# Optimization experiments

Measured on AMD Instinct MI355X. Metric: run time of the kernel, lower is better.

The kernel has to match this reference:

```python
import jax, jax.numpy as jnp
import numpy as np

B = 4096
INPUT_SIZE = 256
LATENT = 64
HIDDEN = 512
ACTIONS = 12
EXPERTS = 8
GATE_H = 128
IN_DIM = INPUT_SIZE + LATENT      # 320, first-layer expert in-dim
INTER = HIDDEN + LATENT           # 576, later-layer expert in-dim


def _lip_linear_params(key, out_f, in_f):
    kw, kb = jax.random.split(key)
    stdv = 1.0 / np.sqrt(in_f)
    W = jax.random.uniform(kw, (out_f, in_f), jnp.float32, -stdv, stdv)
    b = jax.random.uniform(kb, (out_f,), jnp.float32, -stdv, stdv)
    c = jnp.abs(W).sum(1).max()[None]  # shape (1,), matches init
    return W, b, c


def _expert_params(key, e, in_f, out_f):
    # kaiming_uniform_ on tensor of shape (E, in, out): fan_in computed by torch
    kw = key
    gain = np.sqrt(2.0)  # default a=sqrt(5) -> gain = sqrt(2/(1+5)) ... torch uses a=math.sqrt(5)? no: default a=0
    # torch.nn.init.kaiming_uniform_(weight) default a=0, fan_in = in*out? torch computes fan from dims[1:]
    fan_in = in_f
    bound = np.sqrt(6.0 / fan_in)
    W = jax.random.uniform(kw, (e, in_f, out_f), jnp.float32, -bound, bound)
    b = jnp.full((e, out_f), 0.01, jnp.float32)
    return W, b


def setup_inputs() -> dict:
    key = jax.random.key(0)
    ks = jax.random.split(key, 10)
    z = jax.random.normal(ks[0], (B, LATENT), jnp.float32)
    c = jax.random.normal(ks[1], (B, INPUT_SIZE), jnp.float32)
    w0, b0 = _expert_params(ks[2], EXPERTS, IN_DIM, HIDDEN)
    w1, b1 = _expert_params(ks[3], EXPERTS, INTER, HIDDEN)
    w2, b2 = _expert_params(ks[4], EXPERTS, INTER, ACTIONS)
    gw0, gb0, gc0 = _lip_linear_params(ks[5], GATE_H, IN_DIM)
    gw1, gb1, gc1 = _lip_linear_params(ks[6], GATE_H, GATE_H)
    gw2, gb2, gc2 = _lip_linear_params(ks[7], EXPERTS, GATE_H)
    return {"z": z, "c": c, "w0": w0, "b0": b0, "w1": w1, "b1": b1,
            "w2": w2, "b2": b2, "gw0": gw0, "gb0": gb0, "gc0": gc0,
            "gw1": gw1, "gb1": gb1, "gc1": gc1, "gw2": gw2, "gb2": gb2, "gc2": gc2}


def _lip_linear(x, W, b, cc):
    # LipschitzLinear: scale rows of W so row-wise L1 norm <= softplus(c)
    lipc = jax.nn.softplus(cc)                      # (1,)
    scale = jnp.minimum(lipc / jnp.abs(W).sum(1), 1.0)  # (out,)
    return x @ (W * scale[:, None]).T + b


def _moe_forward(z, c, coeff, layers):
    layer_out = c
    for W, bias, act in layers:
        inp = jnp.concatenate([z, layer_out], axis=1)       # (B, in)
        # per-expert GEMM then coefficient mix: avoids (B,in,out) intermediate
        h = jnp.einsum('bi,eio->beo', inp, W)               # (B, E, out)
        out = jnp.einsum('be,beo->bo', coeff, h) + coeff @ bias
        layer_out = jax.nn.elu(out) if act else out
    return layer_out


def reference(z, c, w0, b0, w1, b1, w2, b2,
              gw0, gb0, gc0, gw1, gb1, gc1, gw2, gb2, gc2):
    x = jnp.concatenate([z, c], axis=1)
    h = jax.nn.elu(_lip_linear(x, gw0, gb0, gc0))
    h = jax.nn.elu(_lip_linear(h, gw1, gb1, gc1))
    logits = _lip_linear(h, gw2, gb2, gc2)
    coeff = jax.nn.softmax(logits, axis=1)                  # (B, E)
    layers = [(w0, b0, True), (w1, b1, True), (w2, b2, False)]
    return _moe_forward(z, c, coeff, layers)
```

## Files before the change

kernel.cpp:

```cpp
#include <hip/hip_runtime.h>
#include <hip/hip_bf16.h>
#include <hip/hip_fp16.h>
#include <math.h>

#define BATCH 4096
#define INPUT_SIZE 256
#define LATENT 64
#define HIDDEN 512
#define ACTIONS 12
#define EXPERTS 8
#define GATE_H 128
#define IN_DIM (INPUT_SIZE + LATENT)
#define INTER (HIDDEN + LATENT)

typedef unsigned int u32;
typedef unsigned short u16;
typedef __attribute__((ext_vector_type(8))) short short8;
typedef __attribute__((ext_vector_type(8))) _Float16 f16x8;
typedef __attribute__((ext_vector_type(16))) float f32x16;

__device__ __forceinline__ u16 f2h(float x) { return __half_as_ushort(__float2half(x)); }
__device__ __forceinline__ float h2f(u16 u) { return __half2float(__ushort_as_half(u)); }

__device__ __forceinline__ void gload16(const void* g, void* lds) {
    __builtin_amdgcn_global_load_lds(
        (const __attribute__((address_space(1))) u32*)g,
        (__attribute__((address_space(3))) u32*)lds, 16, 0, 0);
}

#define GS 4
__global__ __launch_bounds__(256) void gate_forward_v4(
    const float* __restrict__ z, const float* __restrict__ c,
    const float* __restrict__ W0t, const float* __restrict__ b0,
    const float* __restrict__ W1t, const float* __restrict__ b1,
    const float* __restrict__ W2t, const float* __restrict__ b2,
    float* __restrict__ coeff) {
    __shared__ float xs[GS][IN_DIM + 2];
    __shared__ float hq[4][GS][GATE_H];
    __shared__ float h1[GS][GATE_H + 1];
    __shared__ float h2[GS][GATE_H + 1];
    __shared__ float red[GS][EXPERTS];

    const int b4 = blockIdx.x * GS;
    const int t = threadIdx.x;
    const int np = t & 63, kq = t >> 6;
    const int n0 = np * 2;

    for (int idx = t; idx < GS * IN_DIM; idx += 256) {
        const int s = idx / IN_DIM, i = idx - s * IN_DIM;
        xs[s][i] = (i < LATENT) ? z[(size_t)(b4 + s) * LATENT + i]
                                : c[(size_t)(b4 + s) * INPUT_SIZE + (i - LATENT)];
    }
    __syncthreads();

    {
        float a0[GS], a1[GS];
        #pragma unroll
        for (int s = 0; s < GS; ++s) { a0[s] = 0.f; a1[s] = 0.f; }
        const int i0 = kq * 80;
        #pragma unroll 8
        for (int i = i0; i < i0 + 80; ++i) {
            const float2 wv2 = *(const float2*)(W0t + (size_t)i * GATE_H + n0);
            #pragma unroll
            for (int s = 0; s < GS; ++s) {
                a0[s] = fmaf(xs[s][i], wv2.x, a0[s]);
                a1[s] = fmaf(xs[s][i], wv2.y, a1[s]);
            }
        }
        #pragma unroll
        for (int s = 0; s < GS; ++s) { hq[kq][s][n0] = a0[s]; hq[kq][s][n0 + 1] = a1[s]; }
    }
    __syncthreads();
    if (kq == 0) {
        #pragma unroll
        for (int s = 0; s < GS; ++s)
            #pragma unroll
            for (int j = 0; j < 2; ++j) {
                const int n = n0 + j;
                const float v = b0[n] + hq[0][s][n] + hq[1][s][n] + hq[2][s][n] + hq[3][s][n];
                h1[s][n] = v > 0.f ? v : expm1f(v);
            }
    }
    __syncthreads();

    {
        float a0[GS], a1[GS];
        #pragma unroll
        for (int s = 0; s < GS; ++s) { a0[s] = 0.f; a1[s] = 0.f; }
        const int i0 = kq * 32;
        #pragma unroll 8
        for (int i = i0; i < i0 + 32; ++i) {
            const float2 wv2 = *(const float2*)(W1t + (size_t)i * GATE_H + n0);
            #pragma unroll
            for (int s = 0; s < GS; ++s) {
                a0[s] = fmaf(h1[s][i], wv2.x, a0[s]);
                a1[s] = fmaf(h1[s][i], wv2.y, a1[s]);
            }
        }
        #pragma unroll
        for (int s = 0; s < GS; ++s) { hq[kq][s][n0] = a0[s]; hq[kq][s][n0 + 1] = a1[s]; }
    }
    __syncthreads();
    if (kq == 0) {
        #pragma unroll
        for (int s = 0; s < GS; ++s)
            #pragma unroll
            for (int j = 0; j < 2; ++j) {
                const int n = n0 + j;
                const float v = b1[n] + hq[0][s][n] + hq[1][s][n] + hq[2][s][n] + hq[3][s][n];
                h2[s][n] = v > 0.f ? v : expm1f(v);
            }
    }
    __syncthreads();

    if (t < GS * EXPERTS) {
        const int s = t >> 3, e = t & 7;
        float acc = b2[e];
        #pragma unroll 8
        for (int i = 0; i < GATE_H; ++i)
            acc = fmaf(h2[s][i], W2t[(size_t)i * EXPERTS + e], acc);
        red[s][e] = acc;
    }
    __syncthreads();
    if (t < GS) {
        float m = red[t][0];
        #pragma unroll
        for (int i = 1; i < EXPERTS; ++i) m = fmaxf(m, red[t][i]);
        float e[EXPERTS];
        float sum = 0.f;
        #pragma unroll
        for (int i = 0; i < EXPERTS; ++i) { e[i] = expf(red[t][i] - m); sum += e[i]; }
        const float inv = 1.f / sum;
        #pragma unroll
        for (int i = 0; i < EXPERTS; ++i)
            coeff[(size_t)(b4 + t) * EXPERTS + i] = e[i] * inv;
    }
}

__global__ __launch_bounds__(256) void pack_all_kernel(
    const float* __restrict__ w0, const float* __restrict__ w1,
    const float* __restrict__ w2,
    const float* __restrict__ z, const float* __restrict__ c,
    u16* __restrict__ Bpk0, u16* __restrict__ Bpk1, u16* __restrict__ Bpk2,
    u16* __restrict__ Apk0, u16* __restrict__ Apk1, u16* __restrict__ Apk2,
    const float* __restrict__ gw0, const float* __restrict__ gc0,
    const float* __restrict__ gw1, const float* __restrict__ gc1,
    const float* __restrict__ gw2, const float* __restrict__ gc2,
    float* __restrict__ gW0t, float* __restrict__ gW1t, float* __restrict__ gW2t) {
    const int t = threadIdx.x, wv = t >> 6, l = t & 63;
    const int x = blockIdx.x, y = blockIdx.y;

    if (y < 33) {
        __shared__ float tile[4][16][33];
        const float* w; u16* Bpk; int IN, OUT, nblk;
        if (y < 16)      { w = w0; Bpk = Bpk0; IN = IN_DIM; OUT = HIDDEN;  nblk = y; }
        else if (y < 32) { w = w1; Bpk = Bpk1; IN = INTER;  OUT = HIDDEN;  nblk = y - 16; }
        else             { w = w2; Bpk = Bpk2; IN = INTER;  OUT = ACTIONS; nblk = 0; }
        const int NK = IN / 16;
        const int e = x, n0 = nblk * 32;
        const int col = l & 31, half = l >> 5;
        char* base = (char*)Bpk + ((size_t)(nblk * EXPERTS + e) * NK) * 1024;

        for (int jj = wv; jj < NK; jj += 4) {
            #pragma unroll
            for (int i = 0; i < 8; ++i) {
                const int r = i * 2 + half;
                float v = 0.f;
                if (n0 + col < OUT) v = w[((size_t)e * IN + jj * 16 + r) * OUT + n0 + col];
                tile[wv][r][col] = v;
            }
            short8 hh;
            #pragma unroll
            for (int i = 0; i < 8; ++i)
                hh[i] = (short)f2h(tile[wv][half * 8 + i][col]);
            *(short8*)(base + (size_t)jj * 1024 + l * 16) = hh;
        }
    } else if (y < 49) {
        constexpr int NK0 = 20, NK1 = 36;
        const int bblk = (y - 33) * 8 + x;
        const int r = l & 31, half = l >> 5;
        const int row = bblk * 32 + r;
        char* base0 = (char*)Apk0 + (size_t)bblk * NK0 * 1024;
        char* base1 = (char*)Apk1 + (size_t)bblk * NK1 * 1024;
        char* base2 = (char*)Apk2 + (size_t)bblk * NK1 * 1024;

        for (int jj = wv; jj < NK0; jj += 4) {
            const int k = jj * 16 + half * 8;
            const float* src = (k < LATENT) ? (z + (size_t)row * LATENT + k)
                                            : (c + (size_t)row * INPUT_SIZE + (k - LATENT));
            short8 hh;
            #pragma unroll
            for (int i = 0; i < 8; ++i) hh[i] = (short)f2h(src[i]);
            *(short8*)(base0 + (size_t)jj * 1024 + l * 16) = hh;
            if (jj < 4) {
                *(short8*)(base1 + (size_t)jj * 1024 + l * 16) = hh;
                *(short8*)(base2 + (size_t)jj * 1024 + l * 16) = hh;
            }
        }
    } else {
        const int row_g = (y - 49) * 32 + x * 4 + wv;
        if (row_g < 264) {
            const float* W; const float* cc; float* Wt; int cols, rows, row;
            if (row_g < 128)      { W = gw0; cc = gc0; Wt = gW0t; cols = IN_DIM; rows = GATE_H; row = row_g; }
            else if (row_g < 256) { W = gw1; cc = gc1; Wt = gW1t; cols = GATE_H; rows = GATE_H; row = row_g - 128; }
            else                  { W = gw2; cc = gc2; Wt = gW2t; cols = GATE_H; rows = EXPERTS; row = row_g - 256; }
            const float* w = W + (size_t)row * cols;
            float s = 0.f;
            for (int i = l; i < cols; i += 64) s += fabsf(w[i]);
            #pragma unroll
            for (int off = 32; off > 0; off >>= 1) s += __shfl_down(s, off, 64);
            s = __shfl(s, 0, 64);
            const float cv = cc[0];
            const float lipc = (cv > 0.f) ? (cv + log1pf(expf(-cv))) : log1pf(expf(cv));
            const float scale = fminf(lipc / s, 1.0f);
            for (int i = l; i < cols; i += 64)
                Wt[(size_t)i * rows + row] = w[i] * scale;
        }
    }
}

template<int NPART>
__global__ __launch_bounds__(256) void reduce_pack_kernel(
    const u16* __restrict__ P16, const float* __restrict__ coeff,
    const float* __restrict__ bias, u16* __restrict__ ApkNext) {
    constexpr int NK = 36;
    __shared__ float biasS[EXPERTS][256];
    __shared__ float coeffS[32][9];
    const int t = threadIdx.x, wv = t >> 6, l = t & 63;
    const int bblk = blockIdx.x, ch = blockIdx.y;
    const int r = l & 31, half = l >> 5;
    const int row = bblk * 32 + r;

    for (int idx = t; idx < EXPERTS * 256; idx += 256)
        biasS[idx >> 8][idx & 255] = bias[(idx >> 8) * HIDDEN + ch * 256 + (idx & 255)];
    for (int idx = t; idx < 32 * 8; idx += 256)
        coeffS[idx >> 3][idx & 7] = coeff[(size_t)(bblk * 32 + (idx >> 3)) * 8 + (idx & 7)];
    __syncthreads();

    char* base = (char*)ApkNext + (size_t)bblk * NK * 1024;
    for (int jj = ch * 16 + wv; jj < ch * 16 + 16; jj += 4) {
        const int cb = jj * 16 + half * 8;
        float v[8];
        #pragma unroll
        for (int i = 0; i < 8; ++i) v[i] = 0.f;
        #pragma unroll
        for (int p = 0; p < NPART; ++p) {
            const short8 q = *(const short8*)(P16 + ((size_t)p * BATCH + row) * HIDDEN + cb);
            #pragma unroll
            for (int i = 0; i < 8; ++i) v[i] += h2f((u16)q[i]);
        }
        #pragma unroll
        for (int e = 0; e < EXPERTS; ++e) {
            const float cv = coeffS[r][e];
            #pragma unroll
            for (int i = 0; i < 8; ++i) v[i] = fmaf(cv, biasS[e][cb - ch * 256 + i], v[i]);
        }
        short8 hh;
        #pragma unroll
        for (int i = 0; i < 8; ++i) {
            const float hv = v[i] > 0.f ? v[i] : expm1f(v[i]);
            hh[i] = (short)f2h(hv);
        }
        *(short8*)(base + (size_t)(4 + jj) * 1024 + l * 16) = hh;
    }
}

__global__ __launch_bounds__(256) void reduce_out_kernel(
    const float* __restrict__ P2, const float* __restrict__ coeff,
    const float* __restrict__ b2, float* __restrict__ out) {
    const int t = threadIdx.x;
    const int bblk = blockIdx.x;
    for (int idx = t; idx < 32 * ACTIONS; idx += 256) {
        const int r = idx / ACTIONS, n = idx % ACTIONS;
        const int row = bblk * 32 + r;
        float s = 0.f;
        #pragma unroll
        for (int p = 0; p < 8; ++p) s += P2[((size_t)p * BATCH + row) * 32 + n];
        const float* cf = coeff + (size_t)row * 8;
        #pragma unroll
        for (int e = 0; e < 8; ++e) s = fmaf(cf[e], b2[e * ACTIONS + n], s);
        out[(size_t)row * ACTIONS + n] = s;
    }
}

template<int NK, bool F16P>
__global__ __launch_bounds__(512) void moe_gemm_big(
    const u16* __restrict__ Apk, const u16* __restrict__ Bpk,
    const float* __restrict__ coeff, void* __restrict__ Pout) {
    constexpr int TOT = NK / 4;

    __shared__ __align__(16) char As[3 * 16384];
    __shared__ float coeffT[2][128];

    const int t = threadIdx.x, wv = t >> 6, l = t & 63;
    const int wr = wv & 1, wc = wv >> 1;

    const int fid = blockIdx.x + 32 * (blockIdx.y + 4 * blockIdx.z);
    const int xcd = fid & 7, idx = fid >> 3;
    const int bx = xcd * 4 + (idx & 3);
    const int yz = idx >> 2;
    const int by = yz & 3, bz = yz >> 2;

    const int b0 = bx * 128;
    const int bblk0 = bx * 4;
    const int nblkg = by * 4 + wc;
    const int part = bz;
    const int estart = part * 2;

    for (int i2 = t; i2 < 2 * 128; i2 += 512)
        coeffT[i2 >> 7][i2 & 127] =
            coeff[(size_t)(b0 + (i2 & 127)) * EXPERTS + estart + (i2 >> 7)];

    const char* Ab = (const char*)Apk;
    const char* Bbase[2];
    #pragma unroll
    for (int e = 0; e < 2; ++e)
        Bbase[e] = (const char*)Bpk +
                   ((size_t)(nblkg * EXPERTS + estart + e) * NK) * 1024 + l * 16;

    f32x16 accE[2][2];
    accE[0][0] = (f32x16)0.f; accE[0][1] = (f32x16)0.f;
    accE[1][0] = (f32x16)0.f; accE[1][1] = (f32x16)0.f;

    f16x8 breg[2][2][4];

    auto stageA = [&](int s) {
        char* dst = As + (s % 3) * 16384;
        #pragma unroll
        for (int q = 0; q < 2; ++q) {
            const int cf = wv * 2 + q, bb = cf >> 2, kq = cf & 3;
            gload16(Ab + ((size_t)(bblk0 + bb) * NK + s * 4 + kq) * 1024 + l * 16,
                    dst + cf * 1024 + l * 16);
        }
    };

    __syncthreads();

    stageA(0);
    #pragma unroll
    for (int e = 0; e < 2; ++e)
        #pragma unroll
        for (int q = 0; q < 4; ++q)
            breg[0][e][q] = *(const f16x8*)(Bbase[e] + (size_t)q * 1024);
    stageA(1);
    #pragma unroll
    for (int e = 0; e < 2; ++e)
        #pragma unroll
        for (int q = 0; q < 4; ++q)
            breg[1][e][q] = *(const f16x8*)(Bbase[e] + (size_t)(4 + q) * 1024);

    #pragma unroll
    for (int s = 0; s < TOT; ++s) {
        if (s == TOT - 1) asm volatile("s_waitcnt vmcnt(0)" ::: "memory");
        else              asm volatile("s_waitcnt vmcnt(10)" ::: "memory");
        __builtin_amdgcn_sched_barrier(0);
        __builtin_amdgcn_s_barrier();
        __builtin_amdgcn_sched_barrier(0);

        if (s + 2 < TOT) stageA(s + 2);

        const char* buf = As + (s % 3) * 16384;
        f16x8 af0[4], af1[4];
        #pragma unroll
        for (int j = 0; j < 4; ++j) {
            af0[j] = *(const f16x8*)(buf + ((wr * 2 + 0) * 4 + j) * 1024 + l * 16);
            af1[j] = *(const f16x8*)(buf + ((wr * 2 + 1) * 4 + j) * 1024 + l * 16);
        }
        #pragma unroll
        for (int e = 0; e < 2; ++e)
            #pragma unroll
            for (int j = 0; j < 4; ++j) {
                accE[e][0] = __builtin_amdgcn_mfma_f32_32x32x16_f16(af0[j], breg[s & 1][e][j], accE[e][0], 0, 0, 0);
                accE[e][1] = __builtin_amdgcn_mfma_f32_32x32x16_f16(af1[j], breg[s & 1][e][j], accE[e][1], 0, 0, 0);
            }
        if (s + 2 < TOT) {
            #pragma unroll
            for (int e = 0; e < 2; ++e)
                #pragma unroll
                for (int q = 0; q < 4; ++q)
                    breg[s & 1][e][q] = *(const f16x8*)(Bbase[e] + (size_t)((s + 2) * 4 + q) * 1024);
        }
    }

    const int ncol = nblkg * 32 + (l & 31);
    #pragma unroll
    for (int m = 0; m < 2; ++m) {
        #pragma unroll
        for (int g = 0; g < 16; ++g) {
            const int rloc = (g & 3) + 8 * (g >> 2) + 4 * (l >> 5);
            const int row = wr * 64 + m * 32 + rloc;
            float v = coeffT[0][row] * accE[0][m][g] + coeffT[1][row] * accE[1][m][g];
            const size_t off = ((size_t)part * BATCH + b0 + row) * HIDDEN + ncol;
            if (F16P) ((u16*)Pout)[off] = f2h(v);
            else      ((float*)Pout)[off] = v;
        }
    }
}

template<int NK, int WN, int EPB, int OUTW, int GX, int GY, int GZ, bool F16P>
__global__ __launch_bounds__(128 * WN) void moe_gemm(
    const u16* __restrict__ Apk, const u16* __restrict__ Bpk,
    const float* __restrict__ coeff, void* __restrict__ Pout) {
    constexpr int TOT = NK / 4;
    constexpr int NWAVE = 2 * WN;
    constexpr int CPW = 16 / NWAVE;
    constexpr int CPX = GX / 8;

    __shared__ __align__(16) char As[3 * 16384];
    __shared__ float coeffT[EPB][128];

    const int t = threadIdx.x, wv = t >> 6, l = t & 63;
    const int wr = wv & 1, wc = wv >> 1;

    const int fid = blockIdx.x + GX * (blockIdx.y + GY * blockIdx.z);
    const int xcd = fid & 7, idx = fid >> 3;
    const int bx = xcd * CPX + (idx % CPX);
    const int yz = idx / CPX;
    const int by = yz % GY, bz = yz / GY;

    const int b0 = bx * 128;
    const int bblk0 = bx * 4;
    const int nblkg = by * WN + wc;
    const int part = bz;
    const int estart = part * EPB;

    for (int idx2 = t; idx2 < EPB * 128; idx2 += 128 * WN)
        coeffT[idx2 >> 7][idx2 & 127] =
            coeff[(size_t)(b0 + (idx2 & 127)) * EXPERTS + estart + (idx2 >> 7)];

    const char* Ab = (const char*)Apk;
    const char* Bbase[EPB];
    #pragma unroll
    for (int e = 0; e < EPB; ++e)
        Bbase[e] = (const char*)Bpk +
                   ((size_t)(nblkg * EXPERTS + estart + e) * NK) * 1024 + l * 16;

    f32x16 accE[EPB][2];
    #pragma unroll
    for (int e = 0; e < EPB; ++e) { accE[e][0] = (f32x16)0.f; accE[e][1] = (f32x16)0.f; }

    f16x8 breg[2][EPB][4];

    auto stageA = [&](int s) {
        char* dst = As + (s % 3) * 16384;
        #pragma unroll
        for (int q = 0; q < CPW; ++q) {
            const int cf = wv * CPW + q, bb = cf >> 2, kq = cf & 3;
            gload16(Ab + ((size_t)(bblk0 + bb) * NK + s * 4 + kq) * 1024 + l * 16,
                    dst + cf * 1024 + l * 16);
        }
    };

    __syncthreads();

    stageA(0);
    #pragma unroll
    for (int e = 0; e < EPB; ++e)
        #pragma unroll
        for (int q = 0; q < 4; ++q)
            breg[0][e][q] = *(const f16x8*)(Bbase[e] + (size_t)q * 1024);
    stageA(1);
    #pragma unroll
    for (int e = 0; e < EPB; ++e)
        #pragma unroll
        for (int q = 0; q < 4; ++q)
            breg[1][e][q] = *(const f16x8*)(Bbase[e] + (size_t)(4 + q) * 1024);

    #pragma unroll
    for (int s = 0; s < TOT; ++s) {
        if (s == TOT - 1) asm volatile("s_waitcnt vmcnt(0)" ::: "memory");
        else              asm volatile("s_waitcnt vmcnt(12)" ::: "memory");
        __builtin_amdgcn_sched_barrier(0);
        __builtin_amdgcn_s_barrier();
        __builtin_amdgcn_sched_barrier(0);

        if (s + 2 < TOT) stageA(s + 2);

        const char* buf = As + (s % 3) * 16384;
        f16x8 af0[4], af1[4];
        #pragma unroll
        for (int j = 0; j < 4; ++j) {
            af0[j] = *(const f16x8*)(buf + ((wr * 2 + 0) * 4 + j) * 1024 + l * 16);
            af1[j] = *(const f16x8*)(buf + ((wr * 2 + 1) * 4 + j) * 1024 + l * 16);
        }
        #pragma unroll
        for (int e = 0; e < EPB; ++e)
            #pragma unroll
            for (int j = 0; j < 4; ++j) {
                accE[e][0] = __builtin_amdgcn_mfma_f32_32x32x16_f16(af0[j], breg[s & 1][e][j], accE[e][0], 0, 0, 0);
                accE[e][1] = __builtin_amdgcn_mfma_f32_32x32x16_f16(af1[j], breg[s & 1][e][j], accE[e][1], 0, 0, 0);
            }
        if (s + 2 < TOT) {
            #pragma unroll
            for (int e = 0; e < EPB; ++e)
                #pragma unroll
                for (int q = 0; q < 4; ++q)
                    breg[s & 1][e][q] = *(const f16x8*)(Bbase[e] + (size_t)((s + 2) * 4 + q) * 1024);
        }
    }

    const int ncol = nblkg * 32 + (l & 31);
    #pragma unroll
    for (int m = 0; m < 2; ++m) {
        #pragma unroll
        for (int g = 0; g < 16; ++g) {
            const int rloc = (g & 3) + 8 * (g >> 2) + 4 * (l >> 5);
            const int row = wr * 64 + m * 32 + rloc;
            float v = 0.f;
            #pragma unroll
            for (int e = 0; e < EPB; ++e) v = fmaf(coeffT[e][row], accE[e][m][g], v);
            const size_t off = ((size_t)part * BATCH + b0 + row) * OUTW + ncol;
            if (F16P) ((u16*)Pout)[off] = f2h(v);
            else      ((float*)Pout)[off] = v;
        }
    }
}

extern "C" void kernel_launch(void* const* d_in, const int* in_sizes, int n_in,
                              void* d_out, int out_size, void* d_ws, size_t ws_size,
                              hipStream_t stream) {
    const float* z   = (const float*)d_in[0];
    const float* c   = (const float*)d_in[1];
    const float* w0  = (const float*)d_in[2];
    const float* b0  = (const float*)d_in[3];
    const float* w1  = (const float*)d_in[4];
    const float* b1  = (const float*)d_in[5];
    const float* w2  = (const float*)d_in[6];
    const float* b2  = (const float*)d_in[7];
    const float* gw0 = (const float*)d_in[8];
    const float* gb0 = (const float*)d_in[9];
    const float* gc0 = (const float*)d_in[10];
    const float* gw1 = (const float*)d_in[11];
    const float* gb1 = (const float*)d_in[12];
    const float* gc1 = (const float*)d_in[13];
    const float* gw2 = (const float*)d_in[14];
    const float* gb2 = (const float*)d_in[15];
    const float* gc2 = (const float*)d_in[16];
    float* out = (float*)d_out;

    char* p = (char*)d_ws;
    float* coeff = (float*)p;  p += (size_t)BATCH * EXPERTS * 4;
    float* gW0t  = (float*)p;  p += (size_t)GATE_H * IN_DIM * 4;
    float* gW1t  = (float*)p;  p += (size_t)GATE_H * GATE_H * 4;
    float* gW2t  = (float*)p;  p += (size_t)EXPERTS * GATE_H * 4;
    u16* Apk0 = (u16*)p;       p += (size_t)128 * 20 * 1024;
    u16* Apk1 = (u16*)p;       p += (size_t)128 * 36 * 1024;
    u16* Apk2 = (u16*)p;       p += (size_t)128 * 36 * 1024;
    u16* Bpk0 = (u16*)p;       p += (size_t)16 * 8 * 20 * 1024;
    u16* Bpk1 = (u16*)p;       p += (size_t)16 * 8 * 36 * 1024;
    u16* Bpk2 = (u16*)p;       p += (size_t)8 * 36 * 1024;
    u16* P16  = (u16*)p;       p += (size_t)4 * BATCH * HIDDEN * 2;
    float* P32 = (float*)P16;

    pack_all_kernel<<<dim3(8, 58), 256, 0, stream>>>(
        w0, w1, w2, z, c, Bpk0, Bpk1, Bpk2, Apk0, Apk1, Apk2,
        gw0, gc0, gw1, gc1, gw2, gc2, gW0t, gW1t, gW2t);

    gate_forward_v4<<<BATCH / GS, 256, 0, stream>>>(z, c, gW0t, gb0, gW1t, gb1,
                                                    gW2t, gb2, coeff);

    moe_gemm_big<20, true><<<dim3(32, 4, 4), 512, 0, stream>>>(
        Apk0, Bpk0, coeff, P16);
    reduce_pack_kernel<4><<<dim3(128, 2), 256, 0, stream>>>(P16, coeff, b0, Apk1);

    moe_gemm_big<36, true><<<dim3(32, 4, 4), 512, 0, stream>>>(
        Apk1, Bpk1, coeff, P16);
    reduce_pack_kernel<4><<<dim3(128, 2), 256, 0, stream>>>(P16, coeff, b1, Apk2);

    moe_gemm<36, 1, 1, 32, 32, 1, 8, false><<<dim3(32, 1, 8), 128, 0, stream>>>(
        Apk2, Bpk2, coeff, P32);
    reduce_out_kernel<<<128, 256, 0, stream>>>(P32, coeff, b2, out);
}
```

Before: 118.3 us.

## Fuse split-K partial reductions into GEMM kernels via last-block atomic counters

Removes the separate reduce_pack and reduce_out kernels. Each GEMM block now writes its partial, bumps an atomic counter for its tile, and the last arriving block sums the partials, adds the bias, applies ELU and packs the next layer's input. The layer GEMM grid is reshaped to 256-thread blocks with twice as many N tiles. This cuts kernel launches and inter-kernel gaps, at the cost of threadfences, atomics and a serial reduction tail in the last block of each tile. The counters are zeroed by an extra row of pack_all_kernel.

```diff
diff --git a/kernel.cpp b/kernel.cpp
--- a/kernel.cpp
+++ b/kernel.cpp
@@ -146,7 +146,8 @@
     const float* __restrict__ gw0, const float* __restrict__ gc0,
     const float* __restrict__ gw1, const float* __restrict__ gc1,
     const float* __restrict__ gw2, const float* __restrict__ gc2,
-    float* __restrict__ gW0t, float* __restrict__ gW1t, float* __restrict__ gW2t) {
+    float* __restrict__ gW0t, float* __restrict__ gW1t, float* __restrict__ gW2t,
+    int* __restrict__ ctrs) {
     const int t = threadIdx.x, wv = t >> 6, l = t & 63;
     const int x = blockIdx.x, y = blockIdx.y;
 
@@ -197,7 +198,7 @@
                 *(short8*)(base2 + (size_t)jj * 1024 + l * 16) = hh;
             }
         }
-    } else {
+    } else if (y < 58) {
         const int row_g = (y - 49) * 32 + x * 4 + wv;
         if (row_g < 264) {
             const float* W; const float* cc; float* Wt; int cols, rows, row;
@@ -216,98 +217,39 @@
             for (int i = l; i < cols; i += 64)
                 Wt[(size_t)i * rows + row] = w[i] * scale;
         }
+    } else {
+        if (x == 0) for (int i = t; i < 544; i += 256) ctrs[i] = 0;
     }
 }
 
-template<int NPART>
-__global__ __launch_bounds__(256) void reduce_pack_kernel(
-    const u16* __restrict__ P16, const float* __restrict__ coeff,
-    const float* __restrict__ bias, u16* __restrict__ ApkNext) {
-    constexpr int NK = 36;
-    __shared__ float biasS[EXPERTS][256];
-    __shared__ float coeffS[32][9];
-    const int t = threadIdx.x, wv = t >> 6, l = t & 63;
-    const int bblk = blockIdx.x, ch = blockIdx.y;
-    const int r = l & 31, half = l >> 5;
-    const int row = bblk * 32 + r;
-
-    for (int idx = t; idx < EXPERTS * 256; idx += 256)
-        biasS[idx >> 8][idx & 255] = bias[(idx >> 8) * HIDDEN + ch * 256 + (idx & 255)];
-    for (int idx = t; idx < 32 * 8; idx += 256)
-        coeffS[idx >> 3][idx & 7] = coeff[(size_t)(bblk * 32 + (idx >> 3)) * 8 + (idx & 7)];
-    __syncthreads();
-
-    char* base = (char*)ApkNext + (size_t)bblk * NK * 1024;
-    for (int jj = ch * 16 + wv; jj < ch * 16 + 16; jj += 4) {
-        const int cb = jj * 16 + half * 8;
-        float v[8];
-        #pragma unroll
-        for (int i = 0; i < 8; ++i) v[i] = 0.f;
-        #pragma unroll
-        for (int p = 0; p < NPART; ++p) {
-            const short8 q = *(const short8*)(P16 + ((size_t)p * BATCH + row) * HIDDEN + cb);
-            #pragma unroll
-            for (int i = 0; i < 8; ++i) v[i] += h2f((u16)q[i]);
-        }
-        #pragma unroll
-        for (int e = 0; e < EXPERTS; ++e) {
-            const float cv = coeffS[r][e];
-            #pragma unroll
-            for (int i = 0; i < 8; ++i) v[i] = fmaf(cv, biasS[e][cb - ch * 256 + i], v[i]);
-        }
-        short8 hh;
-        #pragma unroll
-        for (int i = 0; i < 8; ++i) {
-            const float hv = v[i] > 0.f ? v[i] : expm1f(v[i]);
-            hh[i] = (short)f2h(hv);
-        }
-        *(short8*)(base + (size_t)(4 + jj) * 1024 + l * 16) = hh;
-    }
-}
-
-__global__ __launch_bounds__(256) void reduce_out_kernel(
-    const float* __restrict__ P2, const float* __restrict__ coeff,
-    const float* __restrict__ b2, float* __restrict__ out) {
-    const int t = threadIdx.x;
-    const int bblk = blockIdx.x;
-    for (int idx = t; idx < 32 * ACTIONS; idx += 256) {
-        const int r = idx / ACTIONS, n = idx % ACTIONS;
-        const int row = bblk * 32 + r;
-        float s = 0.f;
-        #pragma unroll
-        for (int p = 0; p < 8; ++p) s += P2[((size_t)p * BATCH + row) * 32 + n];
-        const float* cf = coeff + (size_t)row * 8;
-        #pragma unroll
-        for (int e = 0; e < 8; ++e) s = fmaf(cf[e], b2[e * ACTIONS + n], s);
-        out[(size_t)row * ACTIONS + n] = s;
-    }
-}
-
-template<int NK, bool F16P>
-__global__ __launch_bounds__(512) void moe_gemm_big(
+template<int NK>
+__global__ __launch_bounds__(256) void moe_gemm_rp(
     const u16* __restrict__ Apk, const u16* __restrict__ Bpk,
-    const float* __restrict__ coeff, void* __restrict__ Pout) {
+    const float* __restrict__ coeff, const float* __restrict__ bias,
+    u16* __restrict__ P16, u16* __restrict__ ApkNext, int* __restrict__ ctr) {
     constexpr int TOT = NK / 4;
+    constexpr int GX = 32, GY = 8, GZ = 4;
 
     __shared__ __align__(16) char As[3 * 16384];
     __shared__ float coeffT[2][128];
+    __shared__ int tick;
 
     const int t = threadIdx.x, wv = t >> 6, l = t & 63;
     const int wr = wv & 1, wc = wv >> 1;
 
-    const int fid = blockIdx.x + 32 * (blockIdx.y + 4 * blockIdx.z);
+    const int fid = blockIdx.x + GX * (blockIdx.y + GY * blockIdx.z);
     const int xcd = fid & 7, idx = fid >> 3;
-    const int bx = xcd * 4 + (idx & 3);
-    const int yz = idx >> 2;
-    const int by = yz & 3, bz = yz >> 2;
+    const int bx = xcd * 4 + (idx % 4);
+    const int yz = idx / 4;
+    const int by = yz % GY, bz = yz / GY;
 
     const int b0 = bx * 128;
     const int bblk0 = bx * 4;
-    const int nblkg = by * 4 + wc;
+    const int nblkg = by * 2 + wc;
     const int part = bz;
     const int estart = part * 2;
 
-    for (int i2 = t; i2 < 2 * 128; i2 += 512)
+    for (int i2 = t; i2 < 2 * 128; i2 += 256)
         coeffT[i2 >> 7][i2 & 127] =
             coeff[(size_t)(b0 + (i2 & 127)) * EXPERTS + estart + (i2 >> 7)];
 
@@ -327,8 +269,8 @@
     auto stageA = [&](int s) {
         char* dst = As + (s % 3) * 16384;
         #pragma unroll
-        for (int q = 0; q < 2; ++q) {
-            const int cf = wv * 2 + q, bb = cf >> 2, kq = cf & 3;
+        for (int q = 0; q < 4; ++q) {
+            const int cf = wv * 4 + q, bb = cf >> 2, kq = cf & 3;
             gload16(Ab + ((size_t)(bblk0 + bb) * NK + s * 4 + kq) * 1024 + l * 16,
                     dst + cf * 1024 + l * 16);
         }
@@ -345,123 +287,6 @@
     stageA(1);
     #pragma unroll
     for (int e = 0; e < 2; ++e)
-        #pragma unroll
-        for (int q = 0; q < 4; ++q)
-            breg[1][e][q] = *(const f16x8*)(Bbase[e] + (size_t)(4 + q) * 1024);
-
-    #pragma unroll
-    for (int s = 0; s < TOT; ++s) {
-        if (s == TOT - 1) asm volatile("s_waitcnt vmcnt(0)" ::: "memory");
-        else              asm volatile("s_waitcnt vmcnt(10)" ::: "memory");
-        __builtin_amdgcn_sched_barrier(0);
-        __builtin_amdgcn_s_barrier();
-        __builtin_amdgcn_sched_barrier(0);
-
-        if (s + 2 < TOT) stageA(s + 2);
-
-        const char* buf = As + (s % 3) * 16384;
-        f16x8 af0[4], af1[4];
-        #pragma unroll
-        for (int j = 0; j < 4; ++j) {
-            af0[j] = *(const f16x8*)(buf + ((wr * 2 + 0) * 4 + j) * 1024 + l * 16);
-            af1[j] = *(const f16x8*)(buf + ((wr * 2 + 1) * 4 + j) * 1024 + l * 16);
-        }
-        #pragma unroll
-        for (int e = 0; e < 2; ++e)
-            #pragma unroll
-            for (int j = 0; j < 4; ++j) {
-                accE[e][0] = __builtin_amdgcn_mfma_f32_32x32x16_f16(af0[j], breg[s & 1][e][j], accE[e][0], 0, 0, 0);
-                accE[e][1] = __builtin_amdgcn_mfma_f32_32x32x16_f16(af1[j], breg[s & 1][e][j], accE[e][1], 0, 0, 0);
-            }
-        if (s + 2 < TOT) {
-            #pragma unroll
-            for (int e = 0; e < 2; ++e)
-                #pragma unroll
-                for (int q = 0; q < 4; ++q)
-                    breg[s & 1][e][q] = *(const f16x8*)(Bbase[e] + (size_t)((s + 2) * 4 + q) * 1024);
-        }
-    }
-
-    const int ncol = nblkg * 32 + (l & 31);
-    #pragma unroll
-    for (int m = 0; m < 2; ++m) {
-        #pragma unroll
-        for (int g = 0; g < 16; ++g) {
-            const int rloc = (g & 3) + 8 * (g >> 2) + 4 * (l >> 5);
-            const int row = wr * 64 + m * 32 + rloc;
-            float v = coeffT[0][row] * accE[0][m][g] + coeffT[1][row] * accE[1][m][g];
-            const size_t off = ((size_t)part * BATCH + b0 + row) * HIDDEN + ncol;
-            if (F16P) ((u16*)Pout)[off] = f2h(v);
-            else      ((float*)Pout)[off] = v;
-        }
-    }
-}
-
-template<int NK, int WN, int EPB, int OUTW, int GX, int GY, int GZ, bool F16P>
-__global__ __launch_bounds__(128 * WN) void moe_gemm(
-    const u16* __restrict__ Apk, const u16* __restrict__ Bpk,
-    const float* __restrict__ coeff, void* __restrict__ Pout) {
-    constexpr int TOT = NK / 4;
-    constexpr int NWAVE = 2 * WN;
-    constexpr int CPW = 16 / NWAVE;
-    constexpr int CPX = GX / 8;
-
-    __shared__ __align__(16) char As[3 * 16384];
-    __shared__ float coeffT[EPB][128];
-
-    const int t = threadIdx.x, wv = t >> 6, l = t & 63;
-    const int wr = wv & 1, wc = wv >> 1;
-
-    const int fid = blockIdx.x + GX * (blockIdx.y + GY * blockIdx.z);
-    const int xcd = fid & 7, idx = fid >> 3;
-    const int bx = xcd * CPX + (idx % CPX);
-    const int yz = idx / CPX;
-    const int by = yz % GY, bz = yz / GY;
-
-    const int b0 = bx * 128;
-    const int bblk0 = bx * 4;
-    const int nblkg = by * WN + wc;
-    const int part = bz;
-    const int estart = part * EPB;
-
-    for (int idx2 = t; idx2 < EPB * 128; idx2 += 128 * WN)
-        coeffT[idx2 >> 7][idx2 & 127] =
-            coeff[(size_t)(b0 + (idx2 & 127)) * EXPERTS + estart + (idx2 >> 7)];
-
-    const char* Ab = (const char*)Apk;
-    const char* Bbase[EPB];
-    #pragma unroll
-    for (int e = 0; e < EPB; ++e)
-        Bbase[e] = (const char*)Bpk +
-                   ((size_t)(nblkg * EXPERTS + estart + e) * NK) * 1024 + l * 16;
-
-    f32x16 accE[EPB][2];
-    #pragma unroll
-    for (int e = 0; e < EPB; ++e) { accE[e][0] = (f32x16)0.f; accE[e][1] = (f32x16)0.f; }
-
-    f16x8 breg[2][EPB][4];
-
-    auto stageA = [&](int s) {
-        char* dst = As + (s % 3) * 16384;
-        #pragma unroll
-        for (int q = 0; q < CPW; ++q) {
-            const int cf = wv * CPW + q, bb = cf >> 2, kq = cf & 3;
-            gload16(Ab + ((size_t)(bblk0 + bb) * NK + s * 4 + kq) * 1024 + l * 16,
-                    dst + cf * 1024 + l * 16);
-        }
-    };
-
-    __syncthreads();
-
-    stageA(0);
-    #pragma unroll
-    for (int e = 0; e < EPB; ++e)
-        #pragma unroll
-        for (int q = 0; q < 4; ++q)
-            breg[0][e][q] = *(const f16x8*)(Bbase[e] + (size_t)q * 1024);
-    stageA(1);
-    #pragma unroll
-    for (int e = 0; e < EPB; ++e)
         #pragma unroll
         for (int q = 0; q < 4; ++q)
             breg[1][e][q] = *(const f16x8*)(Bbase[e] + (size_t)(4 + q) * 1024);
@@ -484,7 +309,7 @@
             af1[j] = *(const f16x8*)(buf + ((wr * 2 + 1) * 4 + j) * 1024 + l * 16);
         }
         #pragma unroll
-        for (int e = 0; e < EPB; ++e)
+        for (int e = 0; e < 2; ++e)
             #pragma unroll
             for (int j = 0; j < 4; ++j) {
                 accE[e][0] = __builtin_amdgcn_mfma_f32_32x32x16_f16(af0[j], breg[s & 1][e][j], accE[e][0], 0, 0, 0);
@@ -492,7 +317,7 @@
             }
         if (s + 2 < TOT) {
             #pragma unroll
-            for (int e = 0; e < EPB; ++e)
+            for (int e = 0; e < 2; ++e)
                 #pragma unroll
                 for (int q = 0; q < 4; ++q)
                     breg[s & 1][e][q] = *(const f16x8*)(Bbase[e] + (size_t)((s + 2) * 4 + q) * 1024);
@@ -506,13 +331,165 @@
         for (int g = 0; g < 16; ++g) {
             const int rloc = (g & 3) + 8 * (g >> 2) + 4 * (l >> 5);
             const int row = wr * 64 + m * 32 + rloc;
-            float v = 0.f;
-            #pragma unroll
-            for (int e = 0; e < EPB; ++e) v = fmaf(coeffT[e][row], accE[e][m][g], v);
-            const size_t off = ((size_t)part * BATCH + b0 + row) * OUTW + ncol;
-            if (F16P) ((u16*)Pout)[off] = f2h(v);
-            else      ((float*)Pout)[off] = v;
-        }
+            float v = coeffT[0][row] * accE[0][m][g] + coeffT[1][row] * accE[1][m][g];
+            P16[((size_t)part * BATCH + b0 + row) * HIDDEN + ncol] = f2h(v);
+        }
+    }
+
+    __threadfence();
+    __syncthreads();
+    if (t == 0) tick = atomicAdd(&ctr[bx * GY + by], 1);
+    __syncthreads();
+    if (tick != GZ - 1) return;
+    __threadfence();
+
+    float* coeffS = (float*)As;
+    float* biasS  = (float*)As + 128 * 8;
+    for (int i = t; i < 128 * 8; i += 256)
+        coeffS[i] = coeff[(size_t)(b0 + (i >> 3)) * 8 + (i & 7)];
+    for (int i = t; i < 8 * 64; i += 256)
+        biasS[i] = bias[(i >> 6) * HIDDEN + by * 64 + (i & 63)];
+    __syncthreads();
+
+    const int r = l & 31, half = l >> 5;
+    const int bblk = bblk0 + wv;
+    const int row = bblk * 32 + r;
+    const int rl8 = (wv * 32 + r) * 8;
+    char* basep = (char*)ApkNext + (size_t)bblk * 36 * 1024;
+    #pragma unroll
+    for (int jj2 = 0; jj2 < 4; ++jj2) {
+        const int jj = by * 4 + jj2;
+        const int cb = jj * 16 + half * 8;
+        float v[8];
+        #pragma unroll
+        for (int i = 0; i < 8; ++i) v[i] = 0.f;
+        #pragma unroll
+        for (int p = 0; p < GZ; ++p) {
+            const short8 q = *(const short8*)(P16 + ((size_t)p * BATCH + row) * HIDDEN + cb);
+            #pragma unroll
+            for (int i = 0; i < 8; ++i) v[i] += h2f((u16)q[i]);
+        }
+        const int cl = cb - by * 64;
+        #pragma unroll
+        for (int e = 0; e < EXPERTS; ++e) {
+            const float cv = coeffS[rl8 + e];
+            #pragma unroll
+            for (int i = 0; i < 8; ++i) v[i] = fmaf(cv, biasS[e * 64 + cl + i], v[i]);
+        }
+        short8 hh;
+        #pragma unroll
+        for (int i = 0; i < 8; ++i) {
+            const float hv = v[i] > 0.f ? v[i] : expm1f(v[i]);
+            hh[i] = (short)f2h(hv);
+        }
+        *(short8*)(basep + (size_t)(4 + jj) * 1024 + l * 16) = hh;
+    }
+}
+
+__global__ __launch_bounds__(128) void moe_gemm_l2f(
+    const u16* __restrict__ Apk, const u16* __restrict__ Bpk,
+    const float* __restrict__ coeff, const float* __restrict__ b2,
+    float* __restrict__ P32, float* __restrict__ out, int* __restrict__ ctr) {
+    constexpr int NK = 36, TOT = 9, GX = 32, GZ = 8;
+
+    __shared__ __align__(16) char As[3 * 16384];
+    __shared__ float coeffT[128];
+    __shared__ int tick;
+
+    const int t = threadIdx.x, wv = t >> 6, l = t & 63;
+    const int wr = wv & 1;
+
+    const int fid = blockIdx.x + GX * blockIdx.z;
+    const int xcd = fid & 7, idx = fid >> 3;
+    const int bx = xcd * 4 + (idx % 4);
+    const int part = idx / 4;
+
+    const int b0 = bx * 128;
+    const int bblk0 = bx * 4;
+
+    for (int i2 = t; i2 < 128; i2 += 128)
+        coeffT[i2] = coeff[(size_t)(b0 + i2) * EXPERTS + part];
+
+    const char* Ab = (const char*)Apk;
+    const char* Bb = (const char*)Bpk + ((size_t)part * NK) * 1024 + l * 16;
+
+    f32x16 accE[2];
+    accE[0] = (f32x16)0.f; accE[1] = (f32x16)0.f;
+
+    f16x8 breg[2][4];
+
+    auto stageA = [&](int s) {
+        char* dst = As + (s % 3) * 16384;
+        #pragma unroll
+        for (int q = 0; q < 8; ++q) {
+            const int cf = wv * 8 + q, bb = cf >> 2, kq = cf & 3;
+            gload16(Ab + ((size_t)(bblk0 + bb) * NK + s * 4 + kq) * 1024 + l * 16,
+                    dst + cf * 1024 + l * 16);
+        }
+    };
+    auto bload = [&](int s, int set) {
+        #pragma unroll
+        for (int q = 0; q < 4; ++q)
+            breg[set][q] = *(const f16x8*)(Bb + (size_t)(s * 4 + q) * 1024);
+    };
+
+    __syncthreads();
+    stageA(0); bload(0, 0);
+    stageA(1); bload(1, 1);
+
+    #pragma unroll
+    for (int s = 0; s < TOT; ++s) {
+        if (s == TOT - 1) asm volatile("s_waitcnt vmcnt(0)" ::: "memory");
+        else              asm volatile("s_waitcnt vmcnt(12)" ::: "memory");
+        __builtin_amdgcn_sched_barrier(0);
+        __builtin_amdgcn_s_barrier();
+        __builtin_amdgcn_sched_barrier(0);
+
+        if (s + 2 < TOT) stageA(s + 2);
+
+        const char* buf = As + (s % 3) * 16384;
+        f16x8 af0[4], af1[4];
+        #pragma unroll
+        for (int j = 0; j < 4; ++j) {
+            af0[j] = *(const f16x8*)(buf + ((wr * 2 + 0) * 4 + j) * 1024 + l * 16);
+            af1[j] = *(const f16x8*)(buf + ((wr * 2 + 1) * 4 + j) * 1024 + l * 16);
+        }
+        #pragma unroll
+        for (int j = 0; j < 4; ++j) {
+            accE[0] = __builtin_amdgcn_mfma_f32_32x32x16_f16(af0[j], breg[s & 1][j], accE[0], 0, 0, 0);
+            accE[1] = __builtin_amdgcn_mfma_f32_32x32x16_f16(af1[j], breg[s & 1][j], accE[1], 0, 0, 0);
+        }
+        if (s + 2 < TOT) bload(s + 2, s & 1);
+    }
+
+    const int ncol = l & 31;
+    #pragma unroll
+    for (int m = 0; m < 2; ++m) {
+        #pragma unroll
+        for (int g = 0; g < 16; ++g) {
+            const int rloc = (g & 3) + 8 * (g >> 2) + 4 * (l >> 5);
+            const int row = wr * 64 + m * 32 + rloc;
+            P32[((size_t)part * BATCH + b0 + row) * 32 + ncol] = coeffT[row] * accE[m][g];
+        }
+    }
+
+    __threadfence();
+    __syncthreads();
+    if (t == 0) tick = atomicAdd(&ctr[bx], 1);
+    __syncthreads();
+    if (tick != GZ - 1) return;
+    __threadfence();
+
+    for (int i = t; i < 128 * ACTIONS; i += 128) {
+        const int rloc = i / ACTIONS, n = i % ACTIONS;
+        const int row = b0 + rloc;
+        float s = 0.f;
+        #pragma unroll
+        for (int p = 0; p < 8; ++p) s += P32[((size_t)p * BATCH + row) * 32 + n];
+        const float* cf = coeff + (size_t)row * 8;
+        #pragma unroll
+        for (int e = 0; e < 8; ++e) s = fmaf(cf[e], b2[e * ACTIONS + n], s);
+        out[(size_t)row * ACTIONS + n] = s;
     }
 }
 
@@ -551,23 +528,24 @@
     u16* Bpk2 = (u16*)p;       p += (size_t)8 * 36 * 1024;
     u16* P16  = (u16*)p;       p += (size_t)4 * BATCH * HIDDEN * 2;
     float* P32 = (float*)P16;
-
-    pack_all_kernel<<<dim3(8, 58), 256, 0, stream>>>(
+    int* ctrs = (int*)p;       p += 544 * 4;
+    int* ctr0 = ctrs;
+    int* ctr1 = ctrs + 256;
+    int* ctr2 = ctrs + 512;
+
+    pack_all_kernel<<<dim3(8, 59), 256, 0, stream>>>(
         w0, w1, w2, z, c, Bpk0, Bpk1, Bpk2, Apk0, Apk1, Apk2,
-        gw0, gc0, gw1, gc1, gw2, gc2, gW0t, gW1t, gW2t);
+        gw0, gc0, gw1, gc1, gw2, gc2, gW0t, gW1t, gW2t, ctrs);
 
     gate_forward_v4<<<BATCH / GS, 256, 0, stream>>>(z, c, gW0t, gb0, gW1t, gb1,
                                                     gW2t, gb2, coeff);
 
-    moe_gemm_big<20, true><<<dim3(32, 4, 4), 512, 0, stream>>>(
-        Apk0, Bpk0, coeff, P16);
-    reduce_pack_kernel<4><<<dim3(128, 2), 256, 0, stream>>>(P16, coeff, b0, Apk1);
-
-    moe_gemm_big<36, true><<<dim3(32, 4, 4), 512, 0, stream>>>(
-        Apk1, Bpk1, coeff, P16);
-    reduce_pack_kernel<4><<<dim3(128, 2), 256, 0, stream>>>(P16, coeff, b1, Apk2);
-
-    moe_gemm<36, 1, 1, 32, 32, 1, 8, false><<<dim3(32, 1, 8), 128, 0, stream>>>(
-        Apk2, Bpk2, coeff, P32);
-    reduce_out_kernel<<<128, 256, 0, stream>>>(P32, coeff, b2, out);
+    moe_gemm_rp<20><<<dim3(32, 8, 4), 256, 0, stream>>>(
+        Apk0, Bpk0, coeff, b0, P16, Apk1, ctr0);
+
+    moe_gemm_rp<36><<<dim3(32, 8, 4), 256, 0, stream>>>(
+        Apk1, Bpk1, coeff, b1, P16, Apk2, ctr1);
+
+    moe_gemm_l2f<<<dim3(32, 1, 8), 128, 0, stream>>>(
+        Apk2, Bpk2, coeff, b2, P32, out, ctr2);
 }
```

After: 361.4 us. 205% more time.
